# Kernel tuning notes

Measured on AMD Instinct MI355X. Metric: run time of the kernel, lower is better.

Reference implementation:

```python
import jax, jax.numpy as jnp
import numpy as np

NUM_OBJ_CLS = 151


def setup_inputs() -> dict:
    key = jax.random.key(0)
    ks = jax.random.split(key, 12)
    N, H, E, U, P, R = 6144, 512, 49152, 2048, 4096, 51
    return {
        "edge_ctx": jax.random.normal(ks[0], (N, H), jnp.float32),
        "union_features": jax.random.normal(ks[1], (E, U), jnp.float32),
        "W_post_emb": jax.random.normal(ks[2], (H, 2 * H), jnp.float32) * (H ** -0.5),
        "b_post_emb": jnp.zeros((2 * H,), jnp.float32),
        "W_post_cat": jax.random.normal(ks[3], (2 * H, P), jnp.float32) * ((2 * H) ** -0.5),
        "b_post_cat": jnp.zeros((P,), jnp.float32),
        "W_up": jax.random.normal(ks[4], (U, P), jnp.float32) * (U ** -0.5),
        "b_up": jnp.zeros((P,), jnp.float32),
        "W_rel": jax.random.normal(ks[5], (P, R), jnp.float32) * (P ** -0.5),
        "b_rel": jnp.zeros((R,), jnp.float32),
        "freq_table": jax.random.normal(ks[6], (NUM_OBJ_CLS * NUM_OBJ_CLS, R), jnp.float32),
        "obj_preds": jax.random.randint(ks[7], (N,), 0, NUM_OBJ_CLS, jnp.int64),
        "pair_idx": jax.random.randint(ks[8], (E, 2), 0, N, jnp.int64),
    }


def reference(edge_ctx, union_features, W_post_emb, b_post_emb, W_post_cat,
              b_post_cat, W_up, b_up, W_rel, b_rel, freq_table,
              obj_preds, pair_idx):
    N, H = edge_ctx.shape
    # post_emb -> split into head/tail representations [N, H] each
    edge_rep = (edge_ctx @ W_post_emb + b_post_emb).reshape(N, 2, H)
    head_rep, tail_rep = edge_rep[:, 0], edge_rep[:, 1]
    # gather per-pair head/tail reps and concat -> [E, 2H]
    prod_rep = jnp.concatenate(
        (head_rep[pair_idx[:, 0]], tail_rep[pair_idx[:, 1]]), axis=-1)
    prod_rep = prod_rep @ W_post_cat + b_post_cat            # [E, P]
    # union feature up-projection (union_single_not_match) and gating multiply
    prod_rep = prod_rep * (union_features @ W_up + b_up)     # [E, P]
    rel_dists = prod_rep @ W_rel + b_rel                     # [E, R]
    # frequency-bias lookup indexed by (head_class, tail_class)
    bias_idx = obj_preds[pair_idx[:, 0]] * NUM_OBJ_CLS + obj_preds[pair_idx[:, 1]]
    rel_dists = rel_dists + freq_table[bias_idx]
    return rel_dists
```

## Files before the change

kernel.cpp:

```cpp
#include <hip/hip_runtime.h>

typedef unsigned short u16;
typedef __attribute__((ext_vector_type(4))) float f32x4;
typedef __attribute__((ext_vector_type(4))) u16 u16x4;
typedef __attribute__((ext_vector_type(8))) u16 u16x8;
typedef __attribute__((ext_vector_type(8))) short short8;

__device__ __forceinline__ u16 f2bf(float f) {
  unsigned int u = __builtin_bit_cast(unsigned int, f);
  u += 0x7FFFu + ((u >> 16) & 1u);
  return (u16)(u >> 16);
}
__device__ __forceinline__ float bf2f(u16 b) {
  unsigned int u = ((unsigned int)b) << 16;
  return __builtin_bit_cast(float, u);
}

__device__ __forceinline__ void gld16(const void* g, void* l) {
  __builtin_amdgcn_global_load_lds(
      (const __attribute__((address_space(1))) unsigned int*)g,
      (__attribute__((address_space(3))) unsigned int*)l, 16, 0, 0);
}

template <int N>
__device__ __forceinline__ void boundary() {
  asm volatile("s_waitcnt vmcnt(%0)" ::"n"(N) : "memory");
  __builtin_amdgcn_s_barrier();
  asm volatile("" ::: "memory");
  __builtin_amdgcn_sched_barrier(0);
}


__global__ __launch_bounds__(256) void cvt_f32_bf16(const float* __restrict__ s,
                                                    u16* __restrict__ d, long n4) {
  long stride = (long)gridDim.x * 256;
  for (long i = (long)blockIdx.x * 256 + threadIdx.x; i < n4; i += stride) {
    f32x4 v = *(const f32x4*)(s + i * 4);
    u16x4 o = {f2bf(v.x), f2bf(v.y), f2bf(v.z), f2bf(v.w)};
    *(u16x4*)(d + i * 4) = o;
  }
}

__global__ __launch_bounds__(256) void transpose_f32_bf16(const float* __restrict__ src,
                                                          u16* __restrict__ dst,
                                                          int R, int C, int CP) {
  __shared__ float tile[32][33];
  int r0 = blockIdx.x * 32, c0 = blockIdx.y * 32;
  int tx = threadIdx.x & 31, ty = threadIdx.x >> 5;
#pragma unroll
  for (int i = 0; i < 32; i += 8) {
    int r = r0 + ty + i, c = c0 + tx;
    tile[ty + i][tx] = (r < R && c < C) ? src[(size_t)r * C + c] : 0.f;
  }
  __syncthreads();
#pragma unroll
  for (int i = 0; i < 32; i += 8) {
    int c = c0 + ty + i, r = r0 + tx;
    if (c < CP && r < R) dst[(size_t)c * R + r] = f2bf(tile[tx][ty + i]);
  }
}


template <int NROW>
__device__ __forceinline__ void stage_direct(const u16* __restrict__ src, int ld,
                                             int kcol0, u16* lds, int tid) {
#pragma unroll
  for (int it = 0; it < NROW / 32; ++it) {
    int idx = it * 256 + tid;
    int row = idx >> 3, c = idx & 7;
    int cc = c ^ (row & 7);
    gld16(src + (size_t)row * ld + kcol0 + cc * 8, (char*)lds + idx * 16);
  }
}

template <int MI>
__device__ __forceinline__ void mma_step(const char* As, const char* Bs, int arow0,
                                         int brow0, int lane, f32x4 acc[MI][4]) {
  int r = lane & 15, q = lane >> 4;
#pragma unroll
  for (int ks = 0; ks < 2; ++ks) {
    short8 a[MI], b[4];
#pragma unroll
    for (int i = 0; i < MI; ++i) {
      int row = arow0 + i * 16 + r;
      a[i] = *(const short8*)(As + row * 128 + ((((ks << 2) + q) ^ (row & 7)) << 4));
    }
#pragma unroll
    for (int j = 0; j < 4; ++j) {
      int row = brow0 + j * 16 + r;
      b[j] = *(const short8*)(Bs + row * 128 + ((((ks << 2) + q) ^ (row & 7)) << 4));
    }
#pragma unroll
    for (int i = 0; i < MI; ++i)
#pragma unroll
      for (int j = 0; j < 4; ++j)
        acc[i][j] = __builtin_amdgcn_mfma_f32_16x16x32_bf16(a[i], b[j], acc[i][j], 0, 0, 0);
  }
}


__global__ __launch_bounds__(256) void gemm1(const u16* __restrict__ ec,
                                             const u16* __restrict__ WpeT,
                                             const float* __restrict__ bpe,
                                             u16* __restrict__ head,
                                             u16* __restrict__ tail) {
  __shared__ __align__(16) u16 As[128 * 64];
  __shared__ __align__(16) u16 Bs[128 * 64];
  int tid = threadIdx.x, lane = tid & 63, wave = tid >> 6;
  int wrow = wave >> 1, wcol = wave & 1;
  int m0 = blockIdx.x * 128, n0 = blockIdx.y * 128;
  f32x4 z = {0.f, 0.f, 0.f, 0.f};
  f32x4 acc[4][4];
#pragma unroll
  for (int i = 0; i < 4; ++i)
#pragma unroll
    for (int j = 0; j < 4; ++j) acc[i][j] = z;

  for (int kb = 0; kb < 8; ++kb) {
    stage_direct<128>(ec + (size_t)m0 * 512, 512, kb * 64, As, tid);
    stage_direct<128>(WpeT + (size_t)n0 * 512, 512, kb * 64, Bs, tid);
    __syncthreads();
    mma_step<4>((const char*)As, (const char*)Bs, wrow * 64, wcol * 64, lane, acc);
    __syncthreads();
  }
  int r = lane & 15, q = lane >> 4;
#pragma unroll
  for (int i = 0; i < 4; ++i) {
    int e = m0 + wrow * 64 + i * 16 + q * 4;
#pragma unroll
    for (int j = 0; j < 4; ++j) {
      int c = n0 + wcol * 64 + j * 16 + r;
      float bb = bpe[c];
#pragma unroll
      for (int g = 0; g < 4; ++g) {
        float v = acc[i][j][g] + bb;
        if (c < 512) head[(size_t)(e + g) * 512 + c] = f2bf(v);
        else         tail[(size_t)(e + g) * 512 + (c - 512)] = f2bf(v);
      }
    }
  }
}


__global__ __launch_bounds__(256) void gemm_hp(const u16* __restrict__ A,
                                               const u16* __restrict__ BT,
                                               u16* __restrict__ P) {
  __shared__ __align__(16) u16 As[128 * 64];
  __shared__ __align__(16) u16 Bs[128 * 64];
  int tid = threadIdx.x, lane = tid & 63, wave = tid >> 6;
  int wrow = wave >> 1, wcol = wave & 1;
  int m0 = blockIdx.x * 128, n0 = blockIdx.y * 128;
  f32x4 z = {0.f, 0.f, 0.f, 0.f};
  f32x4 acc[4][4];
#pragma unroll
  for (int i = 0; i < 4; ++i)
#pragma unroll
    for (int j = 0; j < 4; ++j) acc[i][j] = z;

  for (int kb = 0; kb < 8; ++kb) {
    stage_direct<128>(A + (size_t)m0 * 512, 512, kb * 64, As, tid);
    stage_direct<128>(BT + (size_t)n0 * 512, 512, kb * 64, Bs, tid);
    __syncthreads();
    mma_step<4>((const char*)As, (const char*)Bs, wrow * 64, wcol * 64, lane, acc);
    __syncthreads();
  }
  int r = lane & 15, q = lane >> 4;
#pragma unroll
  for (int i = 0; i < 4; ++i) {
    int e = m0 + wrow * 64 + i * 16 + q * 4;
#pragma unroll
    for (int j = 0; j < 4; ++j) {
      int c = n0 + wcol * 64 + j * 16 + r;
#pragma unroll
      for (int g = 0; g < 4; ++g)
        P[(size_t)(e + g) * 4096 + c] = f2bf(acc[i][j][g]);
    }
  }
}


__global__ __launch_bounds__(512, 2) void gemm_union_8ph(
    const u16* __restrict__ U, const u16* __restrict__ WupT,
    const float* __restrict__ bup, const float* __restrict__ bpc,
    const u16* __restrict__ Hp, const u16* __restrict__ Tp,
    const int* __restrict__ pair, u16* __restrict__ T) {
  extern __shared__ __align__(16) u16 lds[];
  const int tid = threadIdx.x, lane = tid & 63, wave = tid >> 6;
  const int wm = wave >> 2, wn = wave & 3;
  const int r = lane & 15, q = lane >> 4;

  int bid = blockIdx.x;
  int swz = (bid & 7) * 384 + (bid >> 3);
  int m0 = (swz >> 4) * 256, n0 = (swz & 15) * 256;

  const u16* Apanel = U + (size_t)m0 * 2048;
  const u16* Bpanel = WupT + (size_t)n0 * 2048;

  f32x4 acc[8][4];
  f32x4 z = {0.f, 0.f, 0.f, 0.f};
#pragma unroll
  for (int i = 0; i < 8; ++i)
#pragma unroll
    for (int j = 0; j < 4; ++j) acc[i][j] = z;

  auto STAGE = [&](int buf, int mat, int kt, int kh) {
    const u16* src = mat ? Bpanel : Apanel;
#pragma unroll
    for (int it = 0; it < 2; ++it) {
      int id = it * 512 + tid;
      int row = id >> 2, c4 = id & 3;
      gld16(src + (size_t)row * 2048 + kt * 64 + kh * 32 + ((c4 ^ ((row >> 1) & 3)) << 3),
            lds + ((((buf << 1) | mat) << 1 | kh) << 13) + id * 8);
    }
  };
  auto GROUP = [&](int kt, int kh) {
    STAGE(kt & 1, 0, kt, kh);
    STAGE(kt & 1, 1, kt, kh);
  };
  auto LDA = [&](int buf, int kh, int mi) -> short8 {
    int row = wm * 128 + mi * 16 + r;
    return *(const short8*)(lds + (((buf << 1) << 1 | kh) << 13) + row * 32 +
                            ((q ^ ((r >> 1) & 3)) << 3));
  };
  auto LDB = [&](int buf, int kh, int nj) -> short8 {
    int row = wn * 64 + nj * 16 + r;
    return *(const short8*)(lds + ((((buf << 1) | 1) << 1 | kh) << 13) + row * 32 +
                            ((q ^ ((r >> 1) & 3)) << 3));
  };

  GROUP(0, 0);
  GROUP(0, 1);
  GROUP(1, 0);
  GROUP(1, 1);
  boundary<12>();

  short8 a[4], b[4];
  const int NT = 32;
  for (int t = 0; t < NT; ++t) {
    int cur = t & 1;
    bool more = (t < NT - 1);

#pragma unroll
    for (int nj = 0; nj < 4; ++nj) b[nj] = LDB(cur, 0, nj);
#pragma unroll
    for (int mi = 0; mi < 4; ++mi) a[mi] = LDA(cur, 0, mi);
    __builtin_amdgcn_s_setprio(1);
#pragma unroll
    for (int mi = 0; mi < 4; ++mi)
#pragma unroll
      for (int nj = 0; nj < 4; ++nj)
        acc[mi][nj] = __builtin_amdgcn_mfma_f32_16x16x32_bf16(a[mi], b[nj], acc[mi][nj], 0, 0, 0);
    __builtin_amdgcn_s_setprio(0);

#pragma unroll
    for (int mi = 0; mi < 4; ++mi) a[mi] = LDA(cur, 0, mi + 4);
    __builtin_amdgcn_s_setprio(1);
#pragma unroll
    for (int mi = 0; mi < 4; ++mi)
#pragma unroll
      for (int nj = 0; nj < 4; ++nj)
        acc[mi + 4][nj] = __builtin_amdgcn_mfma_f32_16x16x32_bf16(a[mi], b[nj], acc[mi + 4][nj], 0, 0, 0);
    __builtin_amdgcn_s_setprio(0);

    if (t == NT - 1) boundary<0>(); else boundary<8>();
    if (t + 2 < NT) GROUP(t + 2, 0);

#pragma unroll
    for (int nj = 0; nj < 4; ++nj) b[nj] = LDB(cur, 1, nj);
#pragma unroll
    for (int mi = 0; mi < 4; ++mi) a[mi] = LDA(cur, 1, mi);
    __builtin_amdgcn_s_setprio(1);
#pragma unroll
    for (int mi = 0; mi < 4; ++mi)
#pragma unroll
      for (int nj = 0; nj < 4; ++nj)
        acc[mi][nj] = __builtin_amdgcn_mfma_f32_16x16x32_bf16(a[mi], b[nj], acc[mi][nj], 0, 0, 0);
    __builtin_amdgcn_s_setprio(0);

#pragma unroll
    for (int mi = 0; mi < 4; ++mi) a[mi] = LDA(cur, 1, mi + 4);
    __builtin_amdgcn_s_setprio(1);
#pragma unroll
    for (int mi = 0; mi < 4; ++mi)
#pragma unroll
      for (int nj = 0; nj < 4; ++nj)
        acc[mi + 4][nj] = __builtin_amdgcn_mfma_f32_16x16x32_bf16(a[mi], b[nj], acc[mi + 4][nj], 0, 0, 0);
    __builtin_amdgcn_s_setprio(0);

    if (more) {
      if (t <= NT - 3) boundary<8>(); else boundary<4>();
      if (t + 2 < NT) GROUP(t + 2, 1);
    }
  }

  __syncthreads();

  u16* Uw = lds + (wave << 13);
#pragma unroll
  for (int mi = 0; mi < 8; ++mi) {
#pragma unroll
    for (int nj = 0; nj < 4; ++nj) {
      int col = nj * 16 + r;
      float bb = bup[n0 + wn * 64 + col];
#pragma unroll
      for (int g = 0; g < 4; ++g) {
        int rw = mi * 16 + q * 4 + g;
        int byte_off = rw * 128 + ((((col >> 3) ^ (rw & 7)) << 4)) + (col & 7) * 2;
        *(u16*)((char*)Uw + byte_off) = f2bf(acc[mi][nj][g] + bb);
      }
    }
  }
  asm volatile("s_waitcnt lgkmcnt(0)" ::: "memory");
  __builtin_amdgcn_sched_barrier(0);

  int c0 = n0 + wn * 64;
#pragma unroll
  for (int rr = 0; rr < 2; ++rr) {
    int lr = lane * 2 + rr;
    int e = m0 + wm * 128 + lr;
    int h = pair[2 * e], tt = pair[2 * e + 1];
    const u16* hp = Hp + (size_t)h * 4096 + c0;
    const u16* tp = Tp + (size_t)tt * 4096 + c0;
    u16* dst = T + (size_t)e * 4096 + c0;
#pragma unroll
    for (int ch = 0; ch < 8; ++ch) {
      u16x8 hv = *(const u16x8*)(hp + ch * 8);
      u16x8 tv = *(const u16x8*)(tp + ch * 8);
      u16x8 uv = *(const u16x8*)((char*)Uw + lr * 128 + ((ch ^ (lr & 7)) << 4));
      u16x8 o;
#pragma unroll
      for (int k = 0; k < 8; ++k) {
        float p = bf2f(hv[k]) + bf2f(tv[k]) + bpc[c0 + ch * 8 + k];
        o[k] = f2bf(bf2f(uv[k]) * p);
      }
      *(u16x8*)(dst + ch * 8) = o;
    }
  }
}


__global__ __launch_bounds__(256) void gemm4(const u16* __restrict__ T,
                                             const u16* __restrict__ WrelT,
                                             const float* __restrict__ brel,
                                             const float* __restrict__ freq,
                                             const int* __restrict__ obj,
                                             const int* __restrict__ pair,
                                             float* __restrict__ out) {
  __shared__ __align__(16) u16 As[128 * 64];
  __shared__ __align__(16) u16 Bs[64 * 64];
  int tid = threadIdx.x, lane = tid & 63, wave = tid >> 6;
  int m0 = blockIdx.x * 128;
  f32x4 z = {0.f, 0.f, 0.f, 0.f};
  f32x4 acc[2][4];
#pragma unroll
  for (int i = 0; i < 2; ++i)
#pragma unroll
    for (int j = 0; j < 4; ++j) acc[i][j] = z;

  for (int kb = 0; kb < 64; ++kb) {
    stage_direct<128>(T + (size_t)m0 * 4096, 4096, kb * 64, As, tid);
    stage_direct<64>(WrelT, 4096, kb * 64, Bs, tid);
    __syncthreads();
    mma_step<2>((const char*)As, (const char*)Bs, wave * 32, 0, lane, acc);
    __syncthreads();
  }
  int r = lane & 15, q = lane >> 4;
#pragma unroll
  for (int i = 0; i < 2; ++i) {
    int e0r = m0 + wave * 32 + i * 16 + q * 4;
#pragma unroll
    for (int j = 0; j < 4; ++j) {
      int c = j * 16 + r;
      if (c < 51) {
        float bb = brel[c];
#pragma unroll
        for (int g = 0; g < 4; ++g) {
          int e = e0r + g;
          int bidx = obj[pair[2 * e]] * 151 + obj[pair[2 * e + 1]];
          out[(size_t)e * 51 + c] = acc[i][j][g] + bb + freq[(size_t)bidx * 51 + c];
        }
      }
    }
  }
}


extern "C" void kernel_launch(void* const* d_in, const int* in_sizes, int n_in,
                              void* d_out, int out_size, void* d_ws, size_t ws_size,
                              hipStream_t stream) {
  const float* edge_ctx = (const float*)d_in[0];
  const float* unionf   = (const float*)d_in[1];
  const float* Wpe      = (const float*)d_in[2];
  const float* bpe      = (const float*)d_in[3];
  const float* Wpc      = (const float*)d_in[4];
  const float* bpc      = (const float*)d_in[5];
  const float* Wup      = (const float*)d_in[6];
  const float* bup      = (const float*)d_in[7];
  const float* Wrel     = (const float*)d_in[8];
  const float* brel     = (const float*)d_in[9];
  const float* freq     = (const float*)d_in[10];
  const int*   obj      = (const int*)d_in[11];
  const int*   pair     = (const int*)d_in[12];
  float* out = (float*)d_out;

  u16* ws = (u16*)d_ws;
  u16* Tb      = ws;
  u16* ub      = ws + 201326592;
  u16* ec      = ws + 301989888;
  u16* head    = ws + 305135616;
  u16* tail    = ws + 308281344;
  u16* WpeT    = ws + 311427072;
  u16* WpcTopT = ws + 311951360;
  u16* WpcBotT = ws + 314048512;
  u16* WupT    = ws + 316145664;
  u16* WrelT   = ws + 324534272;
  u16* Hp      = ws + 324796416;
  u16* Tp      = ws + 349962240;

  cvt_f32_bf16<<<768, 256, 0, stream>>>(edge_ctx, ec, 786432);
  cvt_f32_bf16<<<4096, 256, 0, stream>>>(unionf, ub, 25165824);
  transpose_f32_bf16<<<dim3(16, 32), 256, 0, stream>>>(Wpe, WpeT, 512, 1024, 1024);
  transpose_f32_bf16<<<dim3(16, 128), 256, 0, stream>>>(Wpc, WpcTopT, 512, 4096, 4096);
  transpose_f32_bf16<<<dim3(16, 128), 256, 0, stream>>>(Wpc + (size_t)512 * 4096, WpcBotT, 512, 4096, 4096);
  transpose_f32_bf16<<<dim3(64, 128), 256, 0, stream>>>(Wup, WupT, 2048, 4096, 4096);
  transpose_f32_bf16<<<dim3(128, 2), 256, 0, stream>>>(Wrel, WrelT, 4096, 51, 64);

  gemm1<<<dim3(48, 8), 256, 0, stream>>>(ec, WpeT, bpe, head, tail);
  gemm_hp<<<dim3(48, 32), 256, 0, stream>>>(head, WpcTopT, Hp);
  gemm_hp<<<dim3(48, 32), 256, 0, stream>>>(tail, WpcBotT, Tp);
  gemm_union_8ph<<<3072, 512, 131072, stream>>>(ub, WupT, bup, bpc, Hp, Tp, pair, Tb);
  gemm4<<<dim3(384), 256, 0, stream>>>(Tb, WrelT, brel, freq, obj, pair, out);
}
```

Before: 1.476 ms.

## Switch GEMM main loop to one-tile-ahead prefetch with double-buffered fragments

The main loop now prefetches only one K-tile ahead, issuing both halves at the top of each iteration, instead of keeping two tiles in flight with waits between half-steps. LDS fragment loads are double-buffered in registers (a0/a1, b0/b1) so the next fragment loads overlap the preceding MFMA group. The aim is to cut barrier and waitcnt points per iteration and overlap LDS reads with matrix math. It shortens prefetch distance, so global-load latency may be hidden less, and it raises register pressure.

```diff
diff --git a/kernel.cpp b/kernel.cpp
--- a/kernel.cpp
+++ b/kernel.cpp
@@ -230,67 +230,65 @@
 
   GROUP(0, 0);
   GROUP(0, 1);
-  GROUP(1, 0);
-  GROUP(1, 1);
-  boundary<12>();
-
-  short8 a[4], b[4];
+  boundary<0>();
+
   const int NT = 32;
   for (int t = 0; t < NT; ++t) {
     int cur = t & 1;
     bool more = (t < NT - 1);
 
-#pragma unroll
-    for (int nj = 0; nj < 4; ++nj) b[nj] = LDB(cur, 0, nj);
-#pragma unroll
-    for (int mi = 0; mi < 4; ++mi) a[mi] = LDA(cur, 0, mi);
+    if (more) {
+      GROUP(t + 1, 0);
+      GROUP(t + 1, 1);
+    }
+
+    short8 a0[4], a1[4], b0[4], b1[4];
+#pragma unroll
+    for (int nj = 0; nj < 4; ++nj) b0[nj] = LDB(cur, 0, nj);
+#pragma unroll
+    for (int mi = 0; mi < 4; ++mi) a0[mi] = LDA(cur, 0, mi);
+
+#pragma unroll
+    for (int mi = 0; mi < 4; ++mi) a1[mi] = LDA(cur, 0, mi + 4);
     __builtin_amdgcn_s_setprio(1);
 #pragma unroll
     for (int mi = 0; mi < 4; ++mi)
 #pragma unroll
       for (int nj = 0; nj < 4; ++nj)
-        acc[mi][nj] = __builtin_amdgcn_mfma_f32_16x16x32_bf16(a[mi], b[nj], acc[mi][nj], 0, 0, 0);
+        acc[mi][nj] = __builtin_amdgcn_mfma_f32_16x16x32_bf16(a0[mi], b0[nj], acc[mi][nj], 0, 0, 0);
     __builtin_amdgcn_s_setprio(0);
 
 #pragma unroll
-    for (int mi = 0; mi < 4; ++mi) a[mi] = LDA(cur, 0, mi + 4);
+    for (int nj = 0; nj < 4; ++nj) b1[nj] = LDB(cur, 1, nj);
+#pragma unroll
+    for (int mi = 0; mi < 4; ++mi) a0[mi] = LDA(cur, 1, mi);
     __builtin_amdgcn_s_setprio(1);
 #pragma unroll
     for (int mi = 0; mi < 4; ++mi)
 #pragma unroll
       for (int nj = 0; nj < 4; ++nj)
-        acc[mi + 4][nj] = __builtin_amdgcn_mfma_f32_16x16x32_bf16(a[mi], b[nj], acc[mi + 4][nj], 0, 0, 0);
+        acc[mi + 4][nj] = __builtin_amdgcn_mfma_f32_16x16x32_bf16(a1[mi], b0[nj], acc[mi + 4][nj], 0, 0, 0);
     __builtin_amdgcn_s_setprio(0);
 
-    if (t == NT - 1) boundary<0>(); else boundary<8>();
-    if (t + 2 < NT) GROUP(t + 2, 0);
-
-#pragma unroll
-    for (int nj = 0; nj < 4; ++nj) b[nj] = LDB(cur, 1, nj);
-#pragma unroll
-    for (int mi = 0; mi < 4; ++mi) a[mi] = LDA(cur, 1, mi);
+#pragma unroll
+    for (int mi = 0; mi < 4; ++mi) a1[mi] = LDA(cur, 1, mi + 4);
     __builtin_amdgcn_s_setprio(1);
 #pragma unroll
     for (int mi = 0; mi < 4; ++mi)
 #pragma unroll
       for (int nj = 0; nj < 4; ++nj)
-        acc[mi][nj] = __builtin_amdgcn_mfma_f32_16x16x32_bf16(a[mi], b[nj], acc[mi][nj], 0, 0, 0);
+        acc[mi][nj] = __builtin_amdgcn_mfma_f32_16x16x32_bf16(a0[mi], b1[nj], acc[mi][nj], 0, 0, 0);
     __builtin_amdgcn_s_setprio(0);
 
-#pragma unroll
-    for (int mi = 0; mi < 4; ++mi) a[mi] = LDA(cur, 1, mi + 4);
     __builtin_amdgcn_s_setprio(1);
 #pragma unroll
     for (int mi = 0; mi < 4; ++mi)
 #pragma unroll
       for (int nj = 0; nj < 4; ++nj)
-        acc[mi + 4][nj] = __builtin_amdgcn_mfma_f32_16x16x32_bf16(a[mi], b[nj], acc[mi + 4][nj], 0, 0, 0);
+        acc[mi + 4][nj] = __builtin_amdgcn_mfma_f32_16x16x32_bf16(a1[mi], b1[nj], acc[mi + 4][nj], 0, 0, 0);
     __builtin_amdgcn_s_setprio(0);
 
-    if (more) {
-      if (t <= NT - 3) boundary<8>(); else boundary<4>();
-      if (t + 2 < NT) GROUP(t + 2, 1);
-    }
+    if (more) boundary<0>();
   }
 
   __syncthreads();
```

New measurement: 1.558 ms. +5.6%, slower.
